# Performance work log

Hardware: AMD Instinct MI355X
Metric: run time of the kernel (lower is better)

## Reference

```python
import jax, jax.numpy as jnp
import numpy as np

NUM_DATA, MAX_SEQ_LEN, NUM_INPUTS = 256, 2048, 256
NUM_HIDDEN, NUM_OUTPUTS = 1024, 256

def _xavier(key, shape):
    fan_in, fan_out = shape
    limit = float(np.sqrt(6.0 / (fan_in + fan_out)))
    return jax.random.uniform(key, shape, jnp.float32, -limit, limit)

def setup_inputs() -> dict:
    key = jax.random.key(0)
    ks = jax.random.split(key, 8)
    return {
        "x": jax.random.normal(ks[0], (NUM_DATA, MAX_SEQ_LEN, NUM_INPUTS), jnp.float32),
        "W_in1": _xavier(ks[1], (NUM_INPUTS, NUM_HIDDEN)),
        "b_in1": jnp.zeros((NUM_HIDDEN,), jnp.float32),
        "W_rec1": _xavier(ks[2], (NUM_HIDDEN, NUM_HIDDEN)),
        "W_in2": _xavier(ks[3], (NUM_INPUTS, NUM_HIDDEN)),
        "b_in2": jnp.zeros((NUM_HIDDEN,), jnp.float32),
        "W_rec2": _xavier(ks[4], (NUM_HIDDEN, NUM_HIDDEN)),
        "W_out": _xavier(ks[5], (NUM_HIDDEN, NUM_OUTPUTS)),
        "b_out": jnp.zeros((NUM_OUTPUTS,), jnp.float32),
    }

def reference(x, W_in1, b_in1, W_rec1, W_in2, b_in2, W_rec2, W_out, b_out):
    num_data, max_seq_len, _ = x.shape
    num_hidden = W_in1.shape[1]

    def step_fn(carry, inp):
        z1, z2 = carry                      # each [max_seq_len, num_hidden]
        x_seq, step = inp                   # x_seq: [max_seq_len, num_inputs]
        z12 = z1 + z2
        z1_new = jnp.tanh(x_seq @ W_in1 + z12 @ W_rec1 + b_in1)
        z2_cand = jnp.tanh(x_seq @ W_in2 + z2 @ W_rec2 + b_in2)
        # Layer2 holds previous state on odd steps
        z2_new = jnp.where((step % 2) == 1, z2, z2_cand)
        z_out = jnp.tanh(z1_new @ W_out + b_out)[-1, :]  # [num_outputs]
        return (z1_new, z2_new), z_out

    z0 = jnp.zeros((max_seq_len, num_hidden), x.dtype)
    steps = jnp.arange(num_data)
    _, out = jax.lax.scan(step_fn, (z0, z0), (x, steps))
    return out  # [num_data, num_outputs]
```

## Files before the change

### kernel.cpp

```cpp
#include <hip/hip_runtime.h>
#include <math.h>

#define ND  256
#define SEQ 2048
#define NI  256
#define NH  1024
#define NO  256

#define RB   64
#define RT   1024
#define HPB  16
#define NHP  (NH + 1)

#define XTB  32
#define OTB  8

#define ALF(p)   __hip_atomic_load((p), __ATOMIC_RELAXED, __HIP_MEMORY_SCOPE_AGENT)
#define ASF(p,v) __hip_atomic_store((p), (v), __ATOMIC_RELAXED, __HIP_MEMORY_SCOPE_AGENT)

__global__ void xproj(const float* __restrict__ x,
                      const float* __restrict__ Win1, const float* __restrict__ b1,
                      const float* __restrict__ Win2, const float* __restrict__ b2,
                      float* __restrict__ X1, float* __restrict__ X2) {
    const int   layer = blockIdx.z;
    const int   t0    = blockIdx.y * XTB;
    const int   h     = blockIdx.x * 256 + threadIdx.x;
    const float* W = layer ? Win2 : Win1;
    const float* b = layer ? b2   : b1;
    float*       X = layer ? X2   : X1;

    __shared__ float lx[XTB][NI];
    for (int idx = threadIdx.x; idx < XTB * NI; idx += 256) {
        int r = idx >> 8, c = idx & (NI - 1);
        lx[r][c] = x[(size_t)(t0 + r) * SEQ * NI + (size_t)(SEQ - 1) * NI + c];
    }
    __syncthreads();

    float acc[XTB];
    float bias = b[h];
    #pragma unroll
    for (int r = 0; r < XTB; ++r) acc[r] = bias;

    for (int i = 0; i < NI; ++i) {
        float wv = W[i * NH + h];
        #pragma unroll
        for (int r = 0; r < XTB; ++r) acc[r] += lx[r][i] * wv;
    }
    #pragma unroll
    for (int r = 0; r < XTB; ++r) X[(t0 + r) * NH + h] = acc[r];
}

__launch_bounds__(RT, 1)
__global__ void recur(const float* __restrict__ Wr1, const float* __restrict__ Wr2,
                      const float* __restrict__ X1,  const float* __restrict__ X2,
                      float* Z12, float* Z2, float* Z1hist, int* flags) {
    __shared__ float lW1[HPB][NHP];
    __shared__ float lW2[HPB][NHP];
    __shared__ float sz [2][NH];
    __shared__ float sz2[2][NH];

    const int tid = threadIdx.x;
    const int b   = blockIdx.x;
    const int h0  = b * HPB;

    for (int idx = tid; idx < HPB * NH; idx += RT) {
        int hw = idx & (HPB - 1);
        int k  = idx >> 4;
        lW1[hw][k] = Wr1[(size_t)k * NH + h0 + hw];
        lW2[hw][k] = Wr2[(size_t)k * NH + h0 + hw];
    }
    __syncthreads();

    const int w = tid >> 6;
    const int l = tid & 63;
    const int h = h0 + w;

    float z2h = 0.0f;

    for (int t = 0; t < ND; ++t) {
        const bool even = (t & 1) == 0;
        const int  q    = t >> 1;

        if (t != 0 && w == 0 && l != b) {
            const int* fp = flags + l * 32;
            while (ALF(fp) < t) { }
        }
        __syncthreads();

        float xv1  = X1[t * NH + h];
        float z12v = ALF(Z12 + (t & 1) * NH + tid);
        float xv2 = 0.0f, z2v = 0.0f;
        if (even) {
            xv2 = X2[t * NH + h];
            z2v = ALF(Z2 + (q & 1) * NH + tid);
        }
        sz[t & 1][tid] = z12v;
        if (even) sz2[q & 1][tid] = z2v;
        __syncthreads();

        float r1 = 0.0f, r2 = 0.0f;
        #pragma unroll
        for (int j = 0; j < 16; ++j) {
            int k = l + 64 * j;
            r1 += sz[t & 1][k] * lW1[w][k];
        }
        if (even) {
            #pragma unroll
            for (int j = 0; j < 16; ++j) {
                int k = l + 64 * j;
                r2 += sz2[q & 1][k] * lW2[w][k];
            }
        }
        #pragma unroll
        for (int off = 32; off; off >>= 1) r1 += __shfl_xor(r1, off, 64);
        if (even) {
            #pragma unroll
            for (int off = 32; off; off >>= 1) r2 += __shfl_xor(r2, off, 64);
        }

        if (l == 0) {
            float z1n = tanhf(xv1 + r1);
            if (even) z2h = tanhf(xv2 + r2);
            Z1hist[t * NH + h] = z1n;
            ASF(Z12 + ((t + 1) & 1) * NH + h, z1n + z2h);
            if (even) ASF(Z2 + (((q + 1) & 1)) * NH + h, z2h);
        }

        if (t == ND - 1) break;

        __builtin_amdgcn_s_waitcnt(0);
        __syncthreads();
        if (tid == 0) ASF(flags + b * 32, t + 1);
    }
}

__global__ void outproj(const float* __restrict__ Z1hist,
                        const float* __restrict__ Wout,
                        const float* __restrict__ bout,
                        float* __restrict__ out) {
    const int t0 = blockIdx.x * OTB;
    const int o  = threadIdx.x;

    __shared__ float lz[OTB][NH];
    for (int idx = threadIdx.x; idx < OTB * NH; idx += 256) {
        int r = idx >> 10, c = idx & (NH - 1);
        lz[r][c] = Z1hist[(t0 + r) * NH + c];
    }
    __syncthreads();

    float acc[OTB];
    float bias = bout[o];
    #pragma unroll
    for (int r = 0; r < OTB; ++r) acc[r] = bias;

    for (int hh = 0; hh < NH; ++hh) {
        float wv = Wout[hh * NO + o];
        #pragma unroll
        for (int r = 0; r < OTB; ++r) acc[r] += lz[r][hh] * wv;
    }
    #pragma unroll
    for (int r = 0; r < OTB; ++r) out[(t0 + r) * NO + o] = tanhf(acc[r]);
}

extern "C" void kernel_launch(void* const* d_in, const int* in_sizes, int n_in,
                              void* d_out, int out_size, void* d_ws, size_t ws_size,
                              hipStream_t stream) {
    const float* x     = (const float*)d_in[0];
    const float* Win1  = (const float*)d_in[1];
    const float* b1    = (const float*)d_in[2];
    const float* Wr1   = (const float*)d_in[3];
    const float* Win2  = (const float*)d_in[4];
    const float* b2    = (const float*)d_in[5];
    const float* Wr2   = (const float*)d_in[6];
    const float* Wout  = (const float*)d_in[7];
    const float* bout  = (const float*)d_in[8];
    float* out = (float*)d_out;

    float* ws    = (float*)d_ws;
    float* Z12   = ws;
    float* Z2    = Z12 + 2 * NH;
    int*   flags = (int*)(Z2 + 2 * NH);
    float* Z1h   = (float*)(flags + RB * 32);
    float* X1    = Z1h + ND * NH;
    float* X2    = X1 + ND * NH;

    hipMemsetAsync(Z12, 0, (4 * NH) * sizeof(float) + RB * 32 * sizeof(int), stream);

    dim3 xg(NH / 256, ND / XTB, 2);
    xproj<<<xg, 256, 0, stream>>>(x, Win1, b1, Win2, b2, X1, X2);

    recur<<<RB, RT, 0, stream>>>(Wr1, Wr2, X1, X2, Z12, Z2, Z1h, flags);

    outproj<<<ND / OTB, NO, 0, stream>>>(Z1h, Wout, bout, out);
}
```

Before: 1.586 ms.

## Distribute grid flag polling across threads and replace end-of-step barrier with LDS counter

Each thread now polls only the flag of the block that owns its hidden slice, so it can load that slice of state as soon as the owner is ready, and the extra pre-load barrier is gone. The end-of-step __syncthreads is replaced by an LDS atomic counter that thread 0 spins on before publishing the flag. The z1+z2 sum is formed on read instead of being stored, and the X loads move after the barrier. This aims to shorten the serial latency of each recurrent step, at the cost of more concurrent global polling and a subtler memory-ordering scheme.

```diff
diff --git a/kernel.cpp b/kernel.cpp
--- a/kernel.cpp
+++ b/kernel.cpp
@@ -53,15 +53,18 @@
 __launch_bounds__(RT, 1)
 __global__ void recur(const float* __restrict__ Wr1, const float* __restrict__ Wr2,
                       const float* __restrict__ X1,  const float* __restrict__ X2,
-                      float* Z12, float* Z2, float* Z1hist, int* flags) {
+                      float* Z1b, float* Z2b, float* Z1hist, int* flags) {
     __shared__ float lW1[HPB][NHP];
     __shared__ float lW2[HPB][NHP];
-    __shared__ float sz [2][NH];
+    __shared__ float sz1[2][NH];
     __shared__ float sz2[2][NH];
+    __shared__ int   cnt[2];
 
     const int tid = threadIdx.x;
     const int b   = blockIdx.x;
     const int h0  = b * HPB;
+
+    if (tid < 2) cnt[tid] = 0;
 
     for (int idx = tid; idx < HPB * NH; idx += RT) {
         int hw = idx & (HPB - 1);
@@ -71,66 +74,75 @@
     }
     __syncthreads();
 
-    const int w = tid >> 6;
-    const int l = tid & 63;
-    const int h = h0 + w;
-
-    float z2h = 0.0f;
+    const int w     = tid >> 6;
+    const int l     = tid & 63;
+    const int h     = h0 + w;
+    const int owner = tid >> 4;
 
     for (int t = 0; t < ND; ++t) {
-        const bool even = (t & 1) == 0;
-        const int  q    = t >> 1;
-
-        if (t != 0 && w == 0 && l != b) {
-            const int* fp = flags + l * 32;
+        const bool even   = (t & 1) == 0;
+        const int  q      = t >> 1;
+        const int  s2     = (t == 0) ? 0 : (even ? (q & 1) : ((q + 1) & 1));
+        const bool stage2 = (t == 0) || !even;
+
+        if (t != 0) {
+            const int* fp = flags + owner * 32;
             while (ALF(fp) < t) { }
         }
+        asm volatile("" ::: "memory");
+        float z1v = ALF(Z1b + (t & 1) * NH + tid);
+        float z2v = 0.0f;
+        if (stage2) z2v = ALF(Z2b + s2 * NH + tid);
+        sz1[t & 1][tid] = z1v;
+        if (stage2) sz2[s2][tid] = z2v;
         __syncthreads();
 
-        float xv1  = X1[t * NH + h];
-        float z12v = ALF(Z12 + (t & 1) * NH + tid);
-        float xv2 = 0.0f, z2v = 0.0f;
-        if (even) {
-            xv2 = X2[t * NH + h];
-            z2v = ALF(Z2 + (q & 1) * NH + tid);
-        }
-        sz[t & 1][tid] = z12v;
-        if (even) sz2[q & 1][tid] = z2v;
-        __syncthreads();
-
+        float xv1 = X1[t * NH + h];
+        float xv2 = even ? X2[t * NH + h] : 0.0f;
+
+        const float* z1c = sz1[t & 1];
+        const float* z2c = sz2[s2];
         float r1 = 0.0f, r2 = 0.0f;
         #pragma unroll
         for (int j = 0; j < 16; ++j) {
             int k = l + 64 * j;
-            r1 += sz[t & 1][k] * lW1[w][k];
+            r1 += (z1c[k] + z2c[k]) * lW1[w][k];
         }
         if (even) {
             #pragma unroll
             for (int j = 0; j < 16; ++j) {
                 int k = l + 64 * j;
-                r2 += sz2[q & 1][k] * lW2[w][k];
+                r2 += z2c[k] * lW2[w][k];
             }
         }
         #pragma unroll
-        for (int off = 32; off; off >>= 1) r1 += __shfl_xor(r1, off, 64);
-        if (even) {
-            #pragma unroll
-            for (int off = 32; off; off >>= 1) r2 += __shfl_xor(r2, off, 64);
+        for (int off = 32; off; off >>= 1) {
+            r1 += __shfl_xor(r1, off, 64);
+            if (even) r2 += __shfl_xor(r2, off, 64);
         }
 
         if (l == 0) {
             float z1n = tanhf(xv1 + r1);
-            if (even) z2h = tanhf(xv2 + r2);
             Z1hist[t * NH + h] = z1n;
-            ASF(Z12 + ((t + 1) & 1) * NH + h, z1n + z2h);
-            if (even) ASF(Z2 + (((q + 1) & 1)) * NH + h, z2h);
+            if (t < ND - 1) {
+                ASF(Z1b + ((t + 1) & 1) * NH + h, z1n);
+                if (even) {
+                    float z2h = tanhf(xv2 + r2);
+                    ASF(Z2b + ((q + 1) & 1) * NH + h, z2h);
+                }
+            }
         }
 
         if (t == ND - 1) break;
 
         __builtin_amdgcn_s_waitcnt(0);
-        __syncthreads();
-        if (tid == 0) ASF(flags + b * 32, t + 1);
+        if (l == 0) atomicAdd(&cnt[t & 1], 1);
+        if (tid == 0) {
+            while (__hip_atomic_load(&cnt[t & 1], __ATOMIC_ACQUIRE,
+                                     __HIP_MEMORY_SCOPE_WORKGROUP) != 16) { }
+            cnt[(t & 1) ^ 1] = 0;
+            ASF(flags + b * 32, t + 1);
+        }
     }
 }
 
@@ -177,19 +189,19 @@
     float* out = (float*)d_out;
 
     float* ws    = (float*)d_ws;
-    float* Z12   = ws;
-    float* Z2    = Z12 + 2 * NH;
-    int*   flags = (int*)(Z2 + 2 * NH);
+    float* Z1b   = ws;
+    float* Z2b   = Z1b + 2 * NH;
+    int*   flags = (int*)(Z2b + 2 * NH);
     float* Z1h   = (float*)(flags + RB * 32);
     float* X1    = Z1h + ND * NH;
     float* X2    = X1 + ND * NH;
 
-    hipMemsetAsync(Z12, 0, (4 * NH) * sizeof(float) + RB * 32 * sizeof(int), stream);
+    hipMemsetAsync(Z1b, 0, (4 * NH) * sizeof(float) + RB * 32 * sizeof(int), stream);
 
     dim3 xg(NH / 256, ND / XTB, 2);
     xproj<<<xg, 256, 0, stream>>>(x, Win1, b1, Win2, b2, X1, X2);
 
-    recur<<<RB, RT, 0, stream>>>(Wr1, Wr2, X1, X2, Z12, Z2, Z1h, flags);
+    recur<<<RB, RT, 0, stream>>>(Wr1, Wr2, X1, X2, Z1b, Z2b, Z1h, flags);
 
     outproj<<<ND / OTB, NO, 0, stream>>>(Z1h, Wout, bout, out);
 }
```

Result: no change. 1.601 ms (+1.0%).
